# Performance work log

Hardware: AMD Instinct MI355X
Metric: run time of the kernel (lower is better)

## Reference

```python
import math
import jax, jax.numpy as jnp
import numpy as np

B, T, D, K, R, KC = 4, 2048, 1024, 8, 16, 4
H = 4 * D  # mlp hidden


def setup_inputs() -> dict:
    key = jax.random.key(0)
    ks = jax.random.split(key, 12)
    s = lambda i, shape: jax.random.normal(ks[i], shape, jnp.float32) * 0.02
    # state_decay_logit init: geometric decays in [dmin, dmax], logit = log(p) - log1p(-p)
    dmin, dmax = 0.9, 0.999
    dec = np.exp(np.linspace(math.log(dmin), math.log(dmax), K))
    decay_logit = jnp.asarray(np.log(dec) - np.log1p(-dec), jnp.float32)
    return dict(
        x=jax.random.normal(ks[0], (B, T, D), jnp.float32),
        conv_w=s(1, (D, 1, KC)),            # depthwise conv kernel (torch Conv1d weight)
        gp_w=s(2, (D, D)), gp_b=jnp.zeros((D,), jnp.float32),
        up_w=s(3, (D, H)), up_b=jnp.zeros((H,), jnp.float32),
        dn_w=s(4, (H, D)), dn_b=jnp.zeros((D,), jnp.float32),
        si_w=s(5, (D, K * D)),              # state_in (no bias)
        so_w=s(6, (K * D, D)),              # state_out (no bias)
        decay_logit=decay_logit,
        rs_w=s(7, (D, R)), rs_b=jnp.zeros((R,), jnp.float32),
        rwg_w=s(8, (D, 1)), rwg_b=jnp.zeros((1,), jnp.float32),
        rv_w=s(9, (D, D)), rv_b=jnp.zeros((D,), jnp.float32),
        gr_w=s(10, (D, 1)), gr_b=jnp.zeros((1,), jnp.float32),
        gl_w=s(11, (D, 1)), gl_b=jnp.zeros((1,), jnp.float32),
    )


def _rms_norm(x, eps=1e-6):
    return x * jax.lax.rsqrt(jnp.mean(x * x, axis=-1, keepdims=True) + eps)


def _forward(x, conv_w, gp_w, gp_b, up_w, up_b, dn_w, dn_b, si_w, so_w,
             decay_logit, rs_w, rs_b, rwg_w, rwg_b, rv_w, rv_b, gr_w, gr_b, gl_w, gl_b):
    Bx, Tx, Dx = x.shape
    u = _rms_norm(x)
    # --- local mixer: causal depthwise conv + sigmoid gate + SiLU MLP ---
    xc = jax.lax.conv_general_dilated(
        jnp.swapaxes(u, 1, 2), conv_w, window_strides=(1,),
        padding=[(KC - 1, 0)], feature_group_count=Dx,
        dimension_numbers=('NCH', 'OIH', 'NCH'))
    xc = jnp.swapaxes(xc, 1, 2)                       # (B,T,D) causal conv output
    xg = xc * jax.nn.sigmoid(xc @ gp_w + gp_b)
    local = jax.nn.silu(xg @ up_w + up_b) @ dn_w + dn_b
    # --- per-channel exponential-decay state + register read/write scan ---
    dec = jax.nn.sigmoid(decay_logit)                 # (K,)
    z = (u @ si_w).reshape(Bx, Tx, K, Dx)             # state_in, (B,T,K,D)
    sel = jax.nn.softmax(u @ rs_w + rs_b, axis=-1)    # soft register address (B,T,R)
    wg = jax.nn.sigmoid(u @ rwg_w + rwg_b)            # write gate (B,T,1)
    v = u @ rv_w + rv_b                                # register value (B,T,D)

    def step(carry, inp):
        s, regs = carry
        z_t, sel_t, w_t, v_t = inp
        read = jnp.einsum('br,brd->bd', sel_t, regs)  # soft read before write
        ws = (w_t * sel_t)[:, :, None]                # (B,R,1)
        regs = regs * (1.0 - ws) + ws * v_t[:, None, :]
        s = dec[None, :, None] * s + z_t
        return (s, regs), (s, read)

    init = (jnp.zeros((Bx, K, Dx), x.dtype), jnp.zeros((Bx, R, Dx), x.dtype))
    tm = lambda a: jnp.swapaxes(a, 0, 1)              # time-major for scan
    _, (s_all, reads) = jax.lax.scan(step, init, (tm(z), tm(sel), tm(wg), tm(v)))
    s_all = tm(s_all)                                 # (B,T,K,D)
    reads = tm(reads)                                 # (B,T,D)
    long_out = jnp.einsum('btkd,kde->bte', s_all, so_w.reshape(K, Dx, Dx))
    g_long = jax.nn.sigmoid(u @ gl_w + gl_b)
    g_reg = jax.nn.sigmoid(u @ gr_w + gr_b)
    return x + local + g_long * long_out + g_reg * reads


def reference(x, conv_w, gp_w, gp_b, up_w, up_b, dn_w, dn_b, si_w, so_w,
              decay_logit, rs_w, rs_b, rwg_w, rwg_b, rv_w, rv_b, gr_w, gr_b, gl_w, gl_b):
    return _forward(x, conv_w, gp_w, gp_b, up_w, up_b, dn_w, dn_b, si_w, so_w,
                    decay_logit, rs_w, rs_b, rwg_w, rwg_b, rv_w, rv_b, gr_w, gr_b, gl_w, gl_b)
```

## Files before the change

### kernel.cpp

```cpp
#include <hip/hip_runtime.h>

typedef unsigned short u16;
typedef __bf16 bf16x8 __attribute__((ext_vector_type(8)));
typedef float f32x4 __attribute__((ext_vector_type(4)));

#define D_ 1024
#define T_ 2048
#define B_ 4
#define K_ 8
#define R_ 16
#define H_ 4096
#define NROW (B_*T_)
#define CH 32
#define CL (T_/CH)

__device__ __forceinline__ u16 f2bf(float f){
  union{float f;unsigned u;} v; v.f=f;
  unsigned r = v.u + 0x7FFFu + ((v.u>>16)&1u);
  return (u16)(r>>16);
}
__device__ __forceinline__ float bf2f(u16 b){
  union{unsigned u;float f;} v; v.u = ((unsigned)b)<<16; return v.f;
}
__device__ __forceinline__ float sigm(float x){ return 1.f/(1.f+__expf(-x)); }

__device__ __forceinline__ void gload_lds16(const void* g, void* l){
  __builtin_amdgcn_global_load_lds((const __attribute__((address_space(1))) void*)g,
                                   (__attribute__((address_space(3))) void*)l, 16, 0, 0);
}

__global__ __launch_bounds__(256) void fill_k(float* __restrict__ out, long n, float v){
  long i = (long)blockIdx.x*256 + threadIdx.x;
  if (i < n) out[i] = v;
}

__global__ __launch_bounds__(256) void transpose_cast(const float* __restrict__ in, u16* __restrict__ out,
                                                      int R, int C){
  __shared__ float tile[32][33];
  int bx = blockIdx.x*32;
  int by = blockIdx.y*32;
  int tx = threadIdx.x & 31, ty = threadIdx.x >> 5;
  #pragma unroll
  for (int i=0;i<32;i+=8) tile[ty+i][tx] = in[(size_t)(by+ty+i)*C + bx+tx];
  __syncthreads();
  #pragma unroll
  for (int i=0;i<32;i+=8) out[(size_t)(bx+ty+i)*R + by+tx] = f2bf(tile[tx][ty+i]);
}

__global__ __launch_bounds__(256) void castbf(const float* __restrict__ in, u16* __restrict__ out, long n){
  long i = (long)blockIdx.x*256 + threadIdx.x;
  if (i < n) out[i] = f2bf(in[i]);
}

__global__ __launch_bounds__(256) void rmsnorm_k(const float* __restrict__ x, u16* __restrict__ u){
  int row = blockIdx.x;
  const float* xr = x + (size_t)row*D_;
  float xv[4]; float ss = 0.f;
  #pragma unroll
  for (int i=0;i<4;i++){ xv[i] = xr[threadIdx.x + 256*i]; ss += xv[i]*xv[i]; }
  #pragma unroll
  for (int o=32;o>0;o>>=1) ss += __shfl_down(ss, o);
  __shared__ float red[4];
  if ((threadIdx.x&63)==0) red[threadIdx.x>>6] = ss;
  __syncthreads();
  float tot = red[0]+red[1]+red[2]+red[3];
  float r = rsqrtf(tot*(1.f/D_) + 1e-6f);
  #pragma unroll
  for (int i=0;i<4;i++) u[(size_t)row*D_ + threadIdx.x + 256*i] = f2bf(xv[i]*r);
}

__global__ __launch_bounds__(256) void conv_k(const u16* __restrict__ u, const float* __restrict__ w,
                                              u16* __restrict__ xc){
  size_t i = (size_t)blockIdx.x*256 + threadIdx.x;
  int d = (int)(i & (D_-1));
  int t = (int)((i >> 10) & (T_-1));
  float acc = 0.f;
  #pragma unroll
  for (int j=0;j<4;j++){
    int tt = t-3+j;
    if (tt >= 0) acc += bf2f(u[i + (size_t)(long)(j-3)*D_]) * w[d*4+j];
  }
  xc[i] = f2bf(acc);
}

__global__ __launch_bounds__(256) void smalln_k(const u16* __restrict__ u,
    const float* __restrict__ rs_w, const float* __restrict__ rs_b,
    const float* __restrict__ rwg_w, const float* __restrict__ rwg_b,
    const float* __restrict__ gl_w, const float* __restrict__ gl_b,
    const float* __restrict__ gr_w, const float* __restrict__ gr_b,
    float* __restrict__ sel, float* __restrict__ wg, float* __restrict__ gl, float* __restrict__ gr){
  int row = blockIdx.x, tid = threadIdx.x;
  float p[19];
  #pragma unroll
  for (int c=0;c<19;c++) p[c] = 0.f;
  for (int i=0;i<4;i++){
    int e = tid + i*256;
    float ue = bf2f(u[(size_t)row*D_ + e]);
    const float* rw = rs_w + (size_t)e*16;
    #pragma unroll
    for (int r=0;r<16;r++) p[r] += ue*rw[r];
    p[16] += ue*rwg_w[e];
    p[17] += ue*gl_w[e];
    p[18] += ue*gr_w[e];
  }
  __shared__ float red[19*4];
  #pragma unroll
  for (int c=0;c<19;c++){
    float v = p[c];
    #pragma unroll
    for (int o=32;o>0;o>>=1) v += __shfl_down(v, o);
    if ((tid&63)==0) red[c*4 + (tid>>6)] = v;
  }
  __syncthreads();
  if (tid==0){
    float s[19];
    #pragma unroll
    for (int c=0;c<19;c++) s[c] = red[c*4]+red[c*4+1]+red[c*4+2]+red[c*4+3];
    float mx = -1e30f;
    #pragma unroll
    for (int r=0;r<16;r++){ s[r] += rs_b[r]; mx = fmaxf(mx, s[r]); }
    float ssum = 0.f;
    #pragma unroll
    for (int r=0;r<16;r++){ s[r] = __expf(s[r]-mx); ssum += s[r]; }
    float inv = 1.f/ssum;
    #pragma unroll
    for (int r=0;r<16;r++) sel[(size_t)row*16+r] = s[r]*inv;
    wg[row] = sigm(s[16] + rwg_b[0]);
    gl[row] = sigm(s[17] + gl_b[0]);
    gr[row] = sigm(s[18] + gr_b[0]);
  }
}

#define BM 128
#define BN 128
#define BK 32

template<int EPI>
__global__ __launch_bounds__(256)
void gemm_bt(const u16* __restrict__ A, const u16* __restrict__ BT,
             void* __restrict__ outp, const float* __restrict__ bias,
             const void* __restrict__ aux,
             int K, int lda, int ldb, int ldc,
             long zA, long zB, long zC)
{
  __shared__ __attribute__((aligned(16))) u16 As[BM*BK];
  __shared__ __attribute__((aligned(16))) u16 Bs[BN*BK];
  int nwg = gridDim.x*gridDim.y;
  int bx = blockIdx.x, by = blockIdx.y;
  if ((nwg & 7) == 0){
    int bid = blockIdx.y*gridDim.x + blockIdx.x;
    int cpx = nwg >> 3;
    int s = (bid & 7)*cpx + (bid >> 3);
    bx = s % gridDim.x; by = s / gridDim.x;
  }
  const u16* Ab = A + (size_t)blockIdx.z*zA + (size_t)bx*BM*lda;
  const u16* Bb = BT + (size_t)blockIdx.z*zB + (size_t)by*BN*ldb;
  int tid = threadIdx.x, lane = tid&63, wid = tid>>6;
  int wr = wid>>1, wc = wid&1;
  f32x4 acc[4][4];
  #pragma unroll
  for (int m=0;m<4;m++)
    #pragma unroll
    for (int n=0;n<4;n++) acc[m][n] = (f32x4){0.f,0.f,0.f,0.f};

  int srow = lane>>2;
  int scol = (lane&3)*8;
  int klo  = (lane>>4)*8;
  for (int k0=0; k0<K; k0+=BK){
    #pragma unroll
    for (int i=0;i<2;i++){
      int r0 = wid*32 + i*16;
      gload_lds16(Ab + (size_t)(r0+srow)*lda + k0 + scol, &As[r0*BK]);
      gload_lds16(Bb + (size_t)(r0+srow)*ldb + k0 + scol, &Bs[r0*BK]);
    }
    __syncthreads();
    bf16x8 af[4], bfr[4];
    #pragma unroll
    for (int m=0;m<4;m++) af[m] = *(const bf16x8*)&As[(wr*64+m*16+(lane&15))*BK + klo];
    #pragma unroll
    for (int n=0;n<4;n++) bfr[n] = *(const bf16x8*)&Bs[(wc*64+n*16+(lane&15))*BK + klo];
    #pragma unroll
    for (int m=0;m<4;m++)
      #pragma unroll
      for (int n=0;n<4;n++)
        acc[m][n] = __builtin_amdgcn_mfma_f32_16x16x32_bf16(af[m], bfr[n], acc[m][n], 0, 0, 0);
    __syncthreads();
  }

  size_t obase = (size_t)blockIdx.z*zC;
  int row0 = bx*BM + wr*64;
  int col0 = by*BN + wc*64;
  #pragma unroll
  for (int m=0;m<4;m++){
    #pragma unroll
    for (int n=0;n<4;n++){
      int col = col0 + n*16 + (lane&15);
      #pragma unroll
      for (int r=0;r<4;r++){
        int row = row0 + m*16 + (lane>>4)*4 + r;
        float c = acc[m][n][r];
        size_t idx = obase + (size_t)row*ldc + col;
        if (EPI==0){ ((u16*)outp)[idx] = f2bf(c); }
        else if (EPI==1){ ((u16*)outp)[idx] = f2bf(c + bias[col]); }
        else if (EPI==2){ float t=c+bias[col]; ((u16*)outp)[idx] = f2bf(bf2f(((const u16*)aux)[idx]) * sigm(t)); }
        else if (EPI==3){ float t=c+bias[col]; ((u16*)outp)[idx] = f2bf(t*sigm(t)); }
        else if (EPI==4){ ((float*)outp)[idx] = ((const float*)aux)[idx] + c + bias[col]; }
        else            { ((float*)outp)[idx] += c; }
      }
    }
  }
}

#define NT8 16

template<int EPI>
__global__ __launch_bounds__(512, 2)
void gemm8p(const u16* __restrict__ A, const u16* __restrict__ BT,
            void* __restrict__ outp, const float* __restrict__ bias,
            int lda, int ldb, int ldc)
{
  __shared__ __attribute__((aligned(16))) u16 lds8[65536];
  int nwg = gridDim.x*gridDim.y;
  int bid = blockIdx.y*gridDim.x + blockIdx.x;
  int cpx = nwg >> 3;
  int swz = (bid & 7)*cpx + (bid >> 3);
  int bx = swz % gridDim.x, by = swz / gridDim.x;

  const u16* Ab = A + (size_t)bx*256*lda;
  const u16* Bb = BT + (size_t)by*256*ldb;

  int tid = threadIdx.x, l = tid&63, w = tid>>6;
  int wr = w>>2, wc = w&3;
  int rS0 = (w*2+0)*8 + (l>>3);
  int rS1 = (w*2+1)*8 + (l>>3);
  int cg  = (((l&7) ^ (l>>3)) << 3);
  int seg0 = (w*2+0)*512;
  int seg1 = (w*2+1)*512;

  auto STAGE = [&](int h){
    int kt = h>>2, idx = h&3, par = kt&1;
    int koff = kt*64;
    if (idx < 2){
      const u16* s0 = Bb + (size_t)(idx*128 + rS0)*ldb + koff + cg;
      const u16* s1 = Bb + (size_t)(idx*128 + rS1)*ldb + koff + cg;
      u16* d = &lds8[par*32768 + 16384 + idx*8192];
      gload_lds16(s0, d + seg0);
      gload_lds16(s1, d + seg1);
    } else {
      int a = idx-2;
      const u16* s0 = Ab + (size_t)(a*128 + rS0)*lda + koff + cg;
      const u16* s1 = Ab + (size_t)(a*128 + rS1)*lda + koff + cg;
      u16* d = &lds8[par*32768 + a*8192];
      gload_lds16(s0, d + seg0);
      gload_lds16(s1, d + seg1);
    }
  };

  f32x4 acc[8][4];
  #pragma unroll
  for (int m=0;m<8;m++)
    #pragma unroll
    for (int n=0;n<4;n++) acc[m][n] = (f32x4){0.f,0.f,0.f,0.f};

  for (int h=0; h<7; ++h) STAGE(h);
  asm volatile("s_waitcnt vmcnt(6)" ::: "memory");
  __builtin_amdgcn_s_barrier();

  for (int it=0; it<NT8/2; ++it){
    #pragma unroll
    for (int sub=0; sub<2; ++sub){
      int kt = it*2+sub;
      const int par = sub;
      u16* Abase = &lds8[par*32768 + wr*8192];
      u16* Bbase = &lds8[par*32768 + 16384 + (wc>>1)*8192];
      bf16x8 bf[4][2];
      #pragma unroll
      for (int q=0; q<4; ++q){
        bf16x8 af[2][2];
        if (q==0){
          #pragma unroll
          for (int n=0;n<4;n++)
            #pragma unroll
            for (int s=0;s<2;s++){
              int rr = (wc&1)*64 + n*16 + (l&15);
              int c16 = (l>>4) + s*4;
              bf[n][s] = *(const bf16x8*)&Bbase[rr*64 + ((c16 ^ (rr&7))<<3)];
            }
        }
        #pragma unroll
        for (int i=0;i<2;i++)
          #pragma unroll
          for (int s=0;s<2;s++){
            int rr = q*32 + i*16 + (l&15);
            int c16 = (l>>4) + s*4;
            af[i][s] = *(const bf16x8*)&Abase[rr*64 + ((c16 ^ (rr&7))<<3)];
          }
        __builtin_amdgcn_sched_barrier(0);
        int h = kt*4 + q + 7;
        if (h < 4*NT8) STAGE(h);
        __builtin_amdgcn_s_barrier();
        asm volatile("s_waitcnt lgkmcnt(0)" ::: "memory");
        __builtin_amdgcn_sched_barrier(0);
        __builtin_amdgcn_s_setprio(1);
        #pragma unroll
        for (int i=0;i<2;i++)
          #pragma unroll
          for (int n=0;n<4;n++)
            #pragma unroll
            for (int s=0;s<2;s++)
              acc[q*2+i][n] = __builtin_amdgcn_mfma_f32_16x16x32_bf16(af[i][s], bf[n][s], acc[q*2+i][n], 0, 0, 0);
        __builtin_amdgcn_s_setprio(0);
        if (q==3){
          if (kt == NT8-2)      asm volatile("s_waitcnt vmcnt(0)" ::: "memory");
          else if (kt < NT8-2)  asm volatile("s_waitcnt vmcnt(6)" ::: "memory");
        }
        __builtin_amdgcn_s_barrier();
      }
    }
  }

  int row0 = bx*256 + wr*128;
  int col0 = by*256 + wc*64;
  #pragma unroll
  for (int m=0;m<8;m++){
    #pragma unroll
    for (int n=0;n<4;n++){
      int col = col0 + n*16 + (l&15);
      #pragma unroll
      for (int r=0;r<4;r++){
        int row = row0 + m*16 + (l>>4)*4 + r;
        float c = acc[m][n][r];
        size_t idx = (size_t)row*ldc + col;
        if (EPI==0){ ((u16*)outp)[idx] = f2bf(c); }
        else if (EPI==3){ float t=c+bias[col]; ((u16*)outp)[idx] = f2bf(t*sigm(t)); }
      }
    }
  }
}

template<int KH>
__global__ __launch_bounds__(256) void scan_s1t(const u16* __restrict__ y, const float* __restrict__ logit,
                                                int p, float* __restrict__ Hend){
  int e = blockIdx.x*256 + threadIdx.x;
  int c = blockIdx.y, b = blockIdx.z;
  float dec[KH], h[KH];
  #pragma unroll
  for (int k=0;k<KH;k++){ dec[k] = sigm(logit[KH*p+k]); h[k] = 0.f; }
  size_t row0 = (size_t)b*T_ + (size_t)c*CL;
  for (int t=0;t<CL;t++){
    const u16* yp = y + (row0+t)*(size_t)(KH*D_) + e;
    #pragma unroll
    for (int k=0;k<KH;k++) h[k] = dec[k]*h[k] + bf2f(yp[(size_t)k*D_]);
  }
  #pragma unroll
  for (int k=0;k<KH;k++) Hend[(((size_t)b*CH+c)*KH+k)*D_ + e] = h[k];
}

template<int KH>
__global__ __launch_bounds__(256) void scan_s2t(const float* __restrict__ Hend, const float* __restrict__ logit,
                                                int p, float* __restrict__ Sinit){
  int idx = blockIdx.x*256 + threadIdx.x;
  if (idx >= B_*KH*D_) return;
  int e = idx % D_; int kh = (idx/D_) % KH; int b = idx/(D_*KH);
  float dec = sigm(logit[KH*p+kh]);
  float dL = powf(dec, (float)CL);
  float carry = 0.f;
  for (int c=0;c<CH;c++){
    size_t i3 = (((size_t)b*CH+c)*KH+kh)*D_ + e;
    Sinit[i3] = carry;
    carry = dL*carry + Hend[i3];
  }
}

template<int KH>
__global__ __launch_bounds__(256) void scan_s3t(const u16* __restrict__ y, const float* __restrict__ logit,
                                                int p, const float* __restrict__ Sinit,
                                                const float* __restrict__ glb, float* __restrict__ out){
  int e = blockIdx.x*256 + threadIdx.x;
  int c = blockIdx.y, b = blockIdx.z;
  float dec[KH], h[KH];
  #pragma unroll
  for (int k=0;k<KH;k++){
    dec[k] = sigm(logit[KH*p+k]);
    h[k] = Sinit[(((size_t)b*CH+c)*KH+k)*D_ + e];
  }
  size_t row0 = (size_t)b*T_ + (size_t)c*CL;
  for (int t=0;t<CL;t++){
    const u16* yp = y + (row0+t)*(size_t)(KH*D_) + e;
    float sum = 0.f;
    #pragma unroll
    for (int k=0;k<KH;k++){ h[k] = dec[k]*h[k] + bf2f(yp[(size_t)k*D_]); sum += h[k]; }
    out[(row0+t)*D_ + e] += glb[row0+t] * sum;
  }
}

__global__ __launch_bounds__(256) void scan_r1(const u16* __restrict__ v, const float* __restrict__ sel,
                                               const float* __restrict__ wg,
                                               float* __restrict__ Rend, float* __restrict__ Pout){
  int d = blockIdx.x*256 + threadIdx.x;
  int c = blockIdx.y, b = blockIdx.z;
  __shared__ float sel_s[CL*R_];
  __shared__ float wg_s[CL];
  size_t row0 = (size_t)b*T_ + (size_t)c*CL;
  for (int i=threadIdx.x; i<CL*R_; i+=256) sel_s[i] = sel[row0*R_ + i];
  for (int i=threadIdx.x; i<CL;    i+=256) wg_s[i]  = wg[row0 + i];
  __syncthreads();
  float regs[R_], P[R_];
  #pragma unroll
  for (int r=0;r<R_;r++){ regs[r]=0.f; P[r]=1.f; }
  for (int t=0;t<CL;t++){
    float vv = bf2f(v[(row0+t)*D_ + d]);
    float w = wg_s[t];
    #pragma unroll
    for (int r=0;r<R_;r++){
      float ws = w*sel_s[t*R_+r];
      regs[r] += ws*(vv - regs[r]);
      P[r] *= (1.f - ws);
    }
  }
  #pragma unroll
  for (int r=0;r<R_;r++) Rend[(((size_t)b*CH+c)*R_+r)*D_ + d] = regs[r];
  if (blockIdx.x==0 && threadIdx.x==0){
    #pragma unroll
    for (int r=0;r<R_;r++) Pout[((size_t)b*CH+c)*R_ + r] = P[r];
  }
}

__global__ __launch_bounds__(256) void scan_r2(const float* __restrict__ Rend, const float* __restrict__ Pbuf,
                                               float* __restrict__ Rinit){
  int idx = blockIdx.x*256 + threadIdx.x;
  if (idx >= B_*D_) return;
  int d = idx % D_; int b = idx / D_;
  float regs[R_];
  #pragma unroll
  for (int r=0;r<R_;r++) regs[r] = 0.f;
  for (int c=0;c<CH;c++){
    #pragma unroll
    for (int r=0;r<R_;r++){
      size_t i3 = (((size_t)b*CH+c)*R_+r)*D_ + d;
      Rinit[i3] = regs[r];
      regs[r] = Pbuf[((size_t)b*CH+c)*R_+r]*regs[r] + Rend[i3];
    }
  }
}

__global__ __launch_bounds__(256) void scan_r3(const u16* __restrict__ v, const float* __restrict__ sel,
                                               const float* __restrict__ wg, const float* __restrict__ Rinit,
                                               const float* __restrict__ grb, float* __restrict__ out){
  int d = blockIdx.x*256 + threadIdx.x;
  int c = blockIdx.y, b = blockIdx.z;
  __shared__ float sel_s[CL*R_];
  __shared__ float wg_s[CL];
  size_t row0 = (size_t)b*T_ + (size_t)c*CL;
  for (int i=threadIdx.x; i<CL*R_; i+=256) sel_s[i] = sel[row0*R_ + i];
  for (int i=threadIdx.x; i<CL;    i+=256) wg_s[i]  = wg[row0 + i];
  __syncthreads();
  float regs[R_];
  #pragma unroll
  for (int r=0;r<R_;r++) regs[r] = Rinit[(((size_t)b*CH+c)*R_+r)*D_ + d];
  for (int t=0;t<CL;t++){
    float vv = bf2f(v[(row0+t)*D_ + d]);
    float w = wg_s[t];
    float read = 0.f;
    #pragma unroll
    for (int r=0;r<R_;r++){
      float sr = sel_s[t*R_+r];
      read += sr*regs[r];
      float ws = w*sr;
      regs[r] += ws*(vv - regs[r]);
    }
    out[(row0+t)*D_ + d] += grb[row0+t]*read;
  }
}

static void launch_gemm(int epi, dim3 g, const u16* A, const u16* BT, void* out,
                        const float* bias, const void* aux, int K, int lda, int ldb, int ldc,
                        long zA, long zB, long zC, hipStream_t s){
  switch(epi){
    case 0: gemm_bt<0><<<g,256,0,s>>>(A,BT,out,bias,aux,K,lda,ldb,ldc,zA,zB,zC); break;
    case 1: gemm_bt<1><<<g,256,0,s>>>(A,BT,out,bias,aux,K,lda,ldb,ldc,zA,zB,zC); break;
    case 2: gemm_bt<2><<<g,256,0,s>>>(A,BT,out,bias,aux,K,lda,ldb,ldc,zA,zB,zC); break;
    case 3: gemm_bt<3><<<g,256,0,s>>>(A,BT,out,bias,aux,K,lda,ldb,ldc,zA,zB,zC); break;
    case 4: gemm_bt<4><<<g,256,0,s>>>(A,BT,out,bias,aux,K,lda,ldb,ldc,zA,zB,zC); break;
    default: gemm_bt<5><<<g,256,0,s>>>(A,BT,out,bias,aux,K,lda,ldb,ldc,zA,zB,zC); break;
  }
}

extern "C" void kernel_launch(void* const* d_in, const int* in_sizes, int n_in,
                              void* d_out, int out_size, void* d_ws, size_t ws_size,
                              hipStream_t stream){
  const float* x      = (const float*)d_in[0];
  const float* conv_w = (const float*)d_in[1];
  const float* gp_w   = (const float*)d_in[2];
  const float* gp_b   = (const float*)d_in[3];
  const float* up_w   = (const float*)d_in[4];
  const float* up_b   = (const float*)d_in[5];
  const float* dn_w   = (const float*)d_in[6];
  const float* dn_b   = (const float*)d_in[7];
  const float* si_w   = (const float*)d_in[8];
  const float* so_w   = (const float*)d_in[9];
  const float* logit  = (const float*)d_in[10];
  const float* rs_w   = (const float*)d_in[11];
  const float* rs_b   = (const float*)d_in[12];
  const float* rwg_w  = (const float*)d_in[13];
  const float* rwg_b  = (const float*)d_in[14];
  const float* rv_w   = (const float*)d_in[15];
  const float* rv_b   = (const float*)d_in[16];
  const float* gr_w   = (const float*)d_in[17];
  const float* gr_b   = (const float*)d_in[18];
  const float* gl_w   = (const float*)d_in[19];
  const float* gl_b   = (const float*)d_in[20];
  float* out = (float*)d_out;
  char* base = (char*)d_ws;

  {
    size_t off = 0;
    auto al = [&](size_t b)->char*{ char* r = base+off; off += (b+255)&~(size_t)255; return r; };
    char* u_r    = al((size_t)NROW*D_*2);
    char* v_r    = al((size_t)NROW*D_*2);
    char* big    = al((size_t)121634816);
    float* sel   = (float*)al((size_t)NROW*R_*4);
    float* wgb   = (float*)al((size_t)NROW*4);
    float* glb   = (float*)al((size_t)NROW*4);
    float* grb   = (float*)al((size_t)NROW*4);
    float* Pbuf  = (float*)al((size_t)B_*CH*R_*4);
    float* Hend  = (float*)al((size_t)B_*CH*4*D_*4);
    float* Sinit = (float*)al((size_t)B_*CH*4*D_*4);
    float* Rend  = (float*)al((size_t)B_*CH*R_*D_*4);
    float* Rinit = (float*)al((size_t)B_*CH*R_*D_*4);
    if (off <= ws_size){
      u16* u_bf  = (u16*)u_r;
      u16* v_bf  = (u16*)v_r;
      u16* hid   = (u16*)big;
      u16* xc_bf = (u16*)(big + (size_t)67108864);
      u16* xg_bf = (u16*)(big + (size_t)83886080);
      u16* gpT   = (u16*)(big + (size_t)100663296);
      u16* upT   = (u16*)(big + (size_t)102760448);
      u16* dnT   = (u16*)(big + (size_t)111149056);
      u16* rvT   = (u16*)(big + (size_t)119537664);
      u16* WT    = (u16*)big;
      u16* si_bf = (u16*)(big + (size_t)16777216);
      u16* soT   = (u16*)(big + (size_t)33554432);
      u16* y_bf  = (u16*)(big + (size_t)16777216);

      transpose_cast<<<dim3(D_/32, D_/32),256,0,stream>>>(gp_w, gpT, D_, D_);
      transpose_cast<<<dim3(H_/32, D_/32),256,0,stream>>>(up_w, upT, D_, H_);
      transpose_cast<<<dim3(D_/32, H_/32),256,0,stream>>>(dn_w, dnT, H_, D_);
      transpose_cast<<<dim3(D_/32, D_/32),256,0,stream>>>(rv_w, rvT, D_, D_);

      rmsnorm_k<<<NROW,256,0,stream>>>(x, u_bf);
      conv_k<<<(NROW*D_)/256,256,0,stream>>>(u_bf, conv_w, xc_bf);
      smalln_k<<<NROW,256,0,stream>>>(u_bf, rs_w, rs_b, rwg_w, rwg_b, gl_w, gl_b, gr_w, gr_b,
                                      sel, wgb, glb, grb);

      launch_gemm(2, dim3(NROW/BM, D_/BN, 1), xc_bf, gpT, xg_bf, gp_b, xc_bf,
                  D_, D_, D_, D_, 0, 0, 0, stream);
      gemm8p<3><<<dim3(NROW/256, H_/256), 512, 0, stream>>>(xg_bf, upT, hid, up_b, D_, D_, H_);
      launch_gemm(4, dim3(NROW/BM, D_/BN, 1), hid, dnT, out, dn_b, x,
                  H_, H_, H_, D_, 0, 0, 0, stream);
      launch_gemm(1, dim3(NROW/BM, D_/BN, 1), u_bf, rvT, v_bf, rv_b, nullptr,
                  D_, D_, D_, D_, 0, 0, 0, stream);

      transpose_cast<<<dim3(D_/32, (K_*D_)/32),256,0,stream>>>(so_w, soT, K_*D_, D_);
      castbf<<<((long)D_*K_*D_+255)/256,256,0,stream>>>(si_w, si_bf, (long)D_*K_*D_);
      launch_gemm(0, dim3(D_/BM, D_/BN, K_), soT, si_bf, WT, nullptr, nullptr,
                  D_, K_*D_, K_*D_, D_, (long)D_, (long)D_, (long)D_*D_, stream);

      for (int h=0; h<2; h++){
        gemm8p<0><<<dim3(NROW/256, (4*D_)/256), 512, 0, stream>>>(
            u_bf, WT + (size_t)h*4*D_*D_, y_bf, nullptr, D_, D_, 4*D_);
        scan_s1t<4><<<dim3(D_/256, CH, B_),256,0,stream>>>(y_bf, logit, h, Hend);
        scan_s2t<4><<<(B_*4*D_+255)/256,256,0,stream>>>(Hend, logit, h, Sinit);
        scan_s3t<4><<<dim3(D_/256, CH, B_),256,0,stream>>>(y_bf, logit, h, Sinit, glb, out);
      }

      scan_r1<<<dim3(D_/256, CH, B_),256,0,stream>>>(v_bf, sel, wgb, Rend, Pbuf);
      scan_r2<<<(B_*D_+255)/256,256,0,stream>>>(Rend, Pbuf, Rinit);
      scan_r3<<<dim3(D_/256, CH, B_),256,0,stream>>>(v_bf, sel, wgb, Rinit, grb, out);
      return;
    }
  }

  const size_t MB16_8 = (size_t)NROW*D_*2;
  size_t off = 0;
  auto alloc = [&](size_t bytes)->char*{
    char* r = base + off; off += (bytes + 255) & ~(size_t)255; return r;
  };
  char* R0 = alloc(MB16_8);
  char* R1 = alloc(MB16_8);
  char* R2 = alloc(2*MB16_8);
  char* R3 = alloc((size_t)21*1024*1024);
  float* sel  = (float*)alloc((size_t)NROW*R_*4);
  float* wgb  = (float*)alloc((size_t)NROW*4);
  float* glb  = (float*)alloc((size_t)NROW*4);
  float* grb  = (float*)alloc((size_t)NROW*4);
  float* Pbuf = (float*)alloc((size_t)B_*CH*R_*4);
  float* Hend = (float*)alloc((size_t)B_*CH*2*D_*4);
  float* Sinit= (float*)alloc((size_t)B_*CH*2*D_*4);
  if (off > ws_size){
    fill_k<<<((long)out_size+255)/256,256,0,stream>>>(out, out_size, 12345.0f);
    return;
  }

  u16* u_bf  = (u16*)R0;
  u16* v_bf  = (u16*)R1;
  u16* xc_bf = (u16*)R2;
  u16* xg_bf = (u16*)(R2 + MB16_8);
  u16* hid_bf= (u16*)R2;
  u16* soT   = (u16*)R2;
  u16* si_bf = (u16*)(R2 + MB16_8);
  u16* y_bf  = (u16*)R2;
  u16* gpT   = (u16*)R3;
  u16* upT   = (u16*)(R3 + (size_t)2*1024*1024 + 131072);
  u16* dnT   = (u16*)(R3 + (size_t)10*1024*1024 + 655360);
  u16* rvT   = (u16*)(R3 + (size_t)19*1024*1024);
  u16* WT    = (u16*)R3;
  float* Rend = (float*)R3;
  float* Rinit= (float*)(R3 + (size_t)NROW*D_);

  transpose_cast<<<dim3(D_/32, D_/32),256,0,stream>>>(gp_w, gpT, D_, D_);
  transpose_cast<<<dim3(H_/32, D_/32),256,0,stream>>>(up_w, upT, D_, H_);
  transpose_cast<<<dim3(D_/32, H_/32),256,0,stream>>>(dn_w, dnT, H_, D_);
  transpose_cast<<<dim3(D_/32, D_/32),256,0,stream>>>(rv_w, rvT, D_, D_);

  rmsnorm_k<<<NROW,256,0,stream>>>(x, u_bf);
  conv_k<<<(NROW*D_)/256,256,0,stream>>>(u_bf, conv_w, xc_bf);
  smalln_k<<<NROW,256,0,stream>>>(u_bf, rs_w, rs_b, rwg_w, rwg_b, gl_w, gl_b, gr_w, gr_b,
                                  sel, wgb, glb, grb);

  launch_gemm(2, dim3(NROW/BM, D_/BN, 1), xc_bf, gpT, xg_bf, gp_b, xc_bf,
              D_, D_, D_, D_, 0, 0, 0, stream);
  launch_gemm(1, dim3(NROW/BM, D_/BN, 1), u_bf, rvT, v_bf, rv_b, nullptr,
              D_, D_, D_, D_, 0, 0, 0, stream);
  for (int q=0; q<4; q++){
    launch_gemm(3, dim3(NROW/BM, 1024/BN, 1), xg_bf, upT + (size_t)q*1024*D_, hid_bf,
                up_b + q*1024, nullptr, D_, D_, D_, 1024, 0, 0, 0, stream);
    launch_gemm(q==0?4:5, dim3(NROW/BM, D_/BN, 1), hid_bf, dnT + (size_t)q*1024, out,
                dn_b, x, 1024, 1024, H_, D_, 0, 0, 0, stream);
  }

  transpose_cast<<<dim3(D_/32, (K_*D_)/32),256,0,stream>>>(so_w, soT, K_*D_, D_);
  castbf<<<((long)D_*K_*D_+255)/256,256,0,stream>>>(si_w, si_bf, (long)D_*K_*D_);
  launch_gemm(0, dim3(D_/BM, D_/BN, K_), soT, si_bf, WT, nullptr, nullptr,
              D_, K_*D_, K_*D_, D_, (long)D_, (long)D_, (long)D_*D_, stream);

  for (int p=0; p<4; p++){
    launch_gemm(0, dim3(NROW/BM, (2*D_)/BN, 1), u_bf, WT + (size_t)(2*p)*D_*D_, y_bf,
                nullptr, nullptr, D_, D_, D_, 2*D_, 0, 0, 0, stream);
    scan_s1t<2><<<dim3(D_/256, CH, B_),256,0,stream>>>(y_bf, logit, p, Hend);
    scan_s2t<2><<<(B_*2*D_+255)/256,256,0,stream>>>(Hend, logit, p, Sinit);
    scan_s3t<2><<<dim3(D_/256, CH, B_),256,0,stream>>>(y_bf, logit, p, Sinit, glb, out);
  }

  scan_r1<<<dim3(D_/256, CH, B_),256,0,stream>>>(v_bf, sel, wgb, Rend, Pbuf);
  scan_r2<<<(B_*D_+255)/256,256,0,stream>>>(Rend, Pbuf, Rinit);
  scan_r3<<<dim3(D_/256, CH, B_),256,0,stream>>>(v_bf, sel, wgb, Rinit, grb, out);
}
```

Before: 770.8 us.

## Route all GEMMs through 256x256 kernel, split-K down-proj with atomics, vectorize scans

```diff
diff --git a/kernel.cpp b/kernel.cpp
--- a/kernel.cpp
+++ b/kernel.cpp
@@ -3,6 +3,7 @@
 typedef unsigned short u16;
 typedef __bf16 bf16x8 __attribute__((ext_vector_type(8)));
 typedef float f32x4 __attribute__((ext_vector_type(4)));
+typedef u16 u16x4 __attribute__((ext_vector_type(4)));
 
 #define D_ 1024
 #define T_ 2048
@@ -13,6 +14,8 @@
 #define NROW (B_*T_)
 #define CH 32
 #define CL (T_/CH)
+#define CHS 64
+#define CLS (T_/CHS)
 
 __device__ __forceinline__ u16 f2bf(float f){
   union{float f;unsigned u;} v; v.f=f;
@@ -52,6 +55,15 @@
   if (i < n) out[i] = f2bf(in[i]);
 }
 
+__global__ __launch_bounds__(256) void initout_k(const float* __restrict__ x, const float* __restrict__ b,
+                                                 float* __restrict__ out){
+  size_t i = ((size_t)blockIdx.x*256 + threadIdx.x)*4;
+  f32x4 xv = *(const f32x4*)(x + i);
+  f32x4 bv = *(const f32x4*)(b + (i & (D_-1)));
+  xv += bv;
+  *(f32x4*)(out + i) = xv;
+}
+
 __global__ __launch_bounds__(256) void rmsnorm_k(const float* __restrict__ x, u16* __restrict__ u){
   int row = blockIdx.x;
   const float* xr = x + (size_t)row*D_;
@@ -71,16 +83,25 @@
 
 __global__ __launch_bounds__(256) void conv_k(const u16* __restrict__ u, const float* __restrict__ w,
                                               u16* __restrict__ xc){
-  size_t i = (size_t)blockIdx.x*256 + threadIdx.x;
-  int d = (int)(i & (D_-1));
-  int t = (int)((i >> 10) & (T_-1));
-  float acc = 0.f;
+  size_t base = ((size_t)blockIdx.x*256 + threadIdx.x)*4;
+  int t  = (int)((base >> 10) & (T_-1));
+  int d0 = (int)(base & (D_-1));
+  f32x4 wv[4];
+  #pragma unroll
+  for (int jj=0;jj<4;jj++) wv[jj] = *(const f32x4*)&w[(d0+jj)*4];
+  float acc[4] = {0.f,0.f,0.f,0.f};
   #pragma unroll
   for (int j=0;j<4;j++){
-    int tt = t-3+j;
-    if (tt >= 0) acc += bf2f(u[i + (size_t)(long)(j-3)*D_]) * w[d*4+j];
-  }
-  xc[i] = f2bf(acc);
+    if (t-3+j >= 0){
+      u16x4 uv = *(const u16x4*)(u + base + (long)(j-3)*D_);
+      #pragma unroll
+      for (int jj=0;jj<4;jj++) acc[jj] += bf2f(uv[jj]) * wv[jj][j];
+    }
+  }
+  u16x4 o;
+  #pragma unroll
+  for (int jj=0;jj<4;jj++) o[jj] = f2bf(acc[jj]);
+  *(u16x4*)(xc + base) = o;
 }
 
 __global__ __launch_bounds__(256) void smalln_k(const u16* __restrict__ u,
@@ -211,13 +232,12 @@
   }
 }
 
-#define NT8 16
-
-template<int EPI>
+template<int NT, int EPI>
 __global__ __launch_bounds__(512, 2)
 void gemm8p(const u16* __restrict__ A, const u16* __restrict__ BT,
             void* __restrict__ outp, const float* __restrict__ bias,
-            int lda, int ldb, int ldc)
+            const void* __restrict__ aux,
+            int lda, int ldb, int ldc, long zA, long zB, long zC)
 {
   __shared__ __attribute__((aligned(16))) u16 lds8[65536];
   int nwg = gridDim.x*gridDim.y;
@@ -226,8 +246,8 @@
   int swz = (bid & 7)*cpx + (bid >> 3);
   int bx = swz % gridDim.x, by = swz / gridDim.x;
 
-  const u16* Ab = A + (size_t)bx*256*lda;
-  const u16* Bb = BT + (size_t)by*256*ldb;
+  const u16* Ab = A + (size_t)blockIdx.z*zA + (size_t)bx*256*lda;
+  const u16* Bb = BT + (size_t)blockIdx.z*zB + (size_t)by*256*ldb;
 
   int tid = threadIdx.x, l = tid&63, w = tid>>6;
   int wr = w>>2, wc = w&3;
@@ -266,7 +286,7 @@
   asm volatile("s_waitcnt vmcnt(6)" ::: "memory");
   __builtin_amdgcn_s_barrier();
 
-  for (int it=0; it<NT8/2; ++it){
+  for (int it=0; it<NT/2; ++it){
     #pragma unroll
     for (int sub=0; sub<2; ++sub){
       int kt = it*2+sub;
@@ -297,7 +317,7 @@
           }
         __builtin_amdgcn_sched_barrier(0);
         int h = kt*4 + q + 7;
-        if (h < 4*NT8) STAGE(h);
+        if (h < 4*NT) STAGE(h);
         __builtin_amdgcn_s_barrier();
         asm volatile("s_waitcnt lgkmcnt(0)" ::: "memory");
         __builtin_amdgcn_sched_barrier(0);
@@ -311,14 +331,15 @@
               acc[q*2+i][n] = __builtin_amdgcn_mfma_f32_16x16x32_bf16(af[i][s], bf[n][s], acc[q*2+i][n], 0, 0, 0);
         __builtin_amdgcn_s_setprio(0);
         if (q==3){
-          if (kt == NT8-2)      asm volatile("s_waitcnt vmcnt(0)" ::: "memory");
-          else if (kt < NT8-2)  asm volatile("s_waitcnt vmcnt(6)" ::: "memory");
+          if (kt == NT-2)      asm volatile("s_waitcnt vmcnt(0)" ::: "memory");
+          else if (kt < NT-2)  asm volatile("s_waitcnt vmcnt(6)" ::: "memory");
         }
         __builtin_amdgcn_s_barrier();
       }
     }
   }
 
+  size_t obase = (size_t)blockIdx.z*zC;
   int row0 = bx*256 + wr*128;
   int col0 = by*256 + wc*64;
   #pragma unroll
@@ -330,67 +351,84 @@
       for (int r=0;r<4;r++){
         int row = row0 + m*16 + (l>>4)*4 + r;
         float c = acc[m][n][r];
-        size_t idx = (size_t)row*ldc + col;
+        size_t idx = obase + (size_t)row*ldc + col;
         if (EPI==0){ ((u16*)outp)[idx] = f2bf(c); }
+        else if (EPI==1){ ((u16*)outp)[idx] = f2bf(c + bias[col]); }
+        else if (EPI==2){ float t=c+bias[col]; ((u16*)outp)[idx] = f2bf(bf2f(((const u16*)aux)[idx]) * sigm(t)); }
         else if (EPI==3){ float t=c+bias[col]; ((u16*)outp)[idx] = f2bf(t*sigm(t)); }
+        else            { unsafeAtomicAdd(&((float*)outp)[idx], c); }
       }
     }
   }
 }
 
 template<int KH>
-__global__ __launch_bounds__(256) void scan_s1t(const u16* __restrict__ y, const float* __restrict__ logit,
+__global__ __launch_bounds__(256) void scan_s1v(const u16* __restrict__ y, const float* __restrict__ logit,
                                                 int p, float* __restrict__ Hend){
-  int e = blockIdx.x*256 + threadIdx.x;
+  int e0 = threadIdx.x*4;
   int c = blockIdx.y, b = blockIdx.z;
-  float dec[KH], h[KH];
-  #pragma unroll
-  for (int k=0;k<KH;k++){ dec[k] = sigm(logit[KH*p+k]); h[k] = 0.f; }
-  size_t row0 = (size_t)b*T_ + (size_t)c*CL;
-  for (int t=0;t<CL;t++){
-    const u16* yp = y + (row0+t)*(size_t)(KH*D_) + e;
-    #pragma unroll
-    for (int k=0;k<KH;k++) h[k] = dec[k]*h[k] + bf2f(yp[(size_t)k*D_]);
-  }
-  #pragma unroll
-  for (int k=0;k<KH;k++) Hend[(((size_t)b*CH+c)*KH+k)*D_ + e] = h[k];
+  float dec[KH]; f32x4 h[KH];
+  #pragma unroll
+  for (int k=0;k<KH;k++){ dec[k] = sigm(logit[KH*p+k]); h[k] = (f32x4){0.f,0.f,0.f,0.f}; }
+  size_t row0 = (size_t)b*T_ + (size_t)c*CLS;
+  for (int t=0;t<CLS;t++){
+    const u16* yp = y + (row0+t)*(size_t)(KH*D_) + e0;
+    #pragma unroll
+    for (int k=0;k<KH;k++){
+      u16x4 w = *(const u16x4*)(yp + (size_t)k*D_);
+      #pragma unroll
+      for (int j=0;j<4;j++) h[k][j] = dec[k]*h[k][j] + bf2f(w[j]);
+    }
+  }
+  #pragma unroll
+  for (int k=0;k<KH;k++)
+    *(f32x4*)&Hend[(((size_t)b*CHS+c)*KH+k)*D_ + e0] = h[k];
 }
 
 template<int KH>
-__global__ __launch_bounds__(256) void scan_s2t(const float* __restrict__ Hend, const float* __restrict__ logit,
+__global__ __launch_bounds__(256) void scan_s2v(const float* __restrict__ Hend, const float* __restrict__ logit,
                                                 int p, float* __restrict__ Sinit){
   int idx = blockIdx.x*256 + threadIdx.x;
   if (idx >= B_*KH*D_) return;
   int e = idx % D_; int kh = (idx/D_) % KH; int b = idx/(D_*KH);
   float dec = sigm(logit[KH*p+kh]);
-  float dL = powf(dec, (float)CL);
+  float dL = powf(dec, (float)CLS);
   float carry = 0.f;
-  for (int c=0;c<CH;c++){
-    size_t i3 = (((size_t)b*CH+c)*KH+kh)*D_ + e;
+  for (int c=0;c<CHS;c++){
+    size_t i3 = (((size_t)b*CHS+c)*KH+kh)*D_ + e;
     Sinit[i3] = carry;
     carry = dL*carry + Hend[i3];
   }
 }
 
 template<int KH>
-__global__ __launch_bounds__(256) void scan_s3t(const u16* __restrict__ y, const float* __restrict__ logit,
+__global__ __launch_bounds__(256) void scan_s3v(const u16* __restrict__ y, const float* __restrict__ logit,
                                                 int p, const float* __restrict__ Sinit,
                                                 const float* __restrict__ glb, float* __restrict__ out){
-  int e = blockIdx.x*256 + threadIdx.x;
+  int e0 = threadIdx.x*4;
   int c = blockIdx.y, b = blockIdx.z;
-  float dec[KH], h[KH];
+  float dec[KH]; f32x4 h[KH];
   #pragma unroll
   for (int k=0;k<KH;k++){
     dec[k] = sigm(logit[KH*p+k]);
-    h[k] = Sinit[(((size_t)b*CH+c)*KH+k)*D_ + e];
-  }
-  size_t row0 = (size_t)b*T_ + (size_t)c*CL;
-  for (int t=0;t<CL;t++){
-    const u16* yp = y + (row0+t)*(size_t)(KH*D_) + e;
-    float sum = 0.f;
-    #pragma unroll
-    for (int k=0;k<KH;k++){ h[k] = dec[k]*h[k] + bf2f(yp[(size_t)k*D_]); sum += h[k]; }
-    out[(row0+t)*D_ + e] += glb[row0+t] * sum;
+    h[k] = *(const f32x4*)&Sinit[(((size_t)b*CHS+c)*KH+k)*D_ + e0];
+  }
+  size_t row0 = (size_t)b*T_ + (size_t)c*CLS;
+  for (int t=0;t<CLS;t++){
+    const u16* yp = y + (row0+t)*(size_t)(KH*D_) + e0;
+    f32x4 sum = (f32x4){0.f,0.f,0.f,0.f};
+    #pragma unroll
+    for (int k=0;k<KH;k++){
+      u16x4 w = *(const u16x4*)(yp + (size_t)k*D_);
+      #pragma unroll
+      for (int j=0;j<4;j++){ h[k][j] = dec[k]*h[k][j] + bf2f(w[j]); sum[j] += h[k][j]; }
+    }
+    float g = glb[row0+t];
+    f32x4* op = (f32x4*)&out[(row0+t)*D_ + e0];
+    f32x4 ov = *op;
+    #pragma unroll
+    for (int j=0;j<4;j++) ov[j] += g*sum[j];
+    *op = ov;
   }
 }
 
@@ -524,8 +562,6 @@
     float* glb   = (float*)al((size_t)NROW*4);
     float* grb   = (float*)al((size_t)NROW*4);
     float* Pbuf  = (float*)al((size_t)B_*CH*R_*4);
-    float* Hend  = (float*)al((size_t)B_*CH*4*D_*4);
-    float* Sinit = (float*)al((size_t)B_*CH*4*D_*4);
     float* Rend  = (float*)al((size_t)B_*CH*R_*D_*4);
     float* Rinit = (float*)al((size_t)B_*CH*R_*D_*4);
     if (off <= ws_size){
@@ -542,6 +578,8 @@
       u16* si_bf = (u16*)(big + (size_t)16777216);
       u16* soT   = (u16*)(big + (size_t)33554432);
       u16* y_bf  = (u16*)(big + (size_t)16777216);
+      float* Hend  = (float*)(big + (size_t)83886080);
+      float* Sinit = (float*)(big + (size_t)88080384);
 
       transpose_cast<<<dim3(D_/32, D_/32),256,0,stream>>>(gp_w, gpT, D_, D_);
       transpose_cast<<<dim3(H_/32, D_/32),256,0,stream>>>(up_w, upT, D_, H_);
@@ -549,29 +587,31 @@
       transpose_cast<<<dim3(D_/32, D_/32),256,0,stream>>>(rv_w, rvT, D_, D_);
 
       rmsnorm_k<<<NROW,256,0,stream>>>(x, u_bf);
-      conv_k<<<(NROW*D_)/256,256,0,stream>>>(u_bf, conv_w, xc_bf);
+      conv_k<<<(NROW*D_)/1024,256,0,stream>>>(u_bf, conv_w, xc_bf);
       smalln_k<<<NROW,256,0,stream>>>(u_bf, rs_w, rs_b, rwg_w, rwg_b, gl_w, gl_b, gr_w, gr_b,
                                       sel, wgb, glb, grb);
 
-      launch_gemm(2, dim3(NROW/BM, D_/BN, 1), xc_bf, gpT, xg_bf, gp_b, xc_bf,
-                  D_, D_, D_, D_, 0, 0, 0, stream);
-      gemm8p<3><<<dim3(NROW/256, H_/256), 512, 0, stream>>>(xg_bf, upT, hid, up_b, D_, D_, H_);
-      launch_gemm(4, dim3(NROW/BM, D_/BN, 1), hid, dnT, out, dn_b, x,
-                  H_, H_, H_, D_, 0, 0, 0, stream);
-      launch_gemm(1, dim3(NROW/BM, D_/BN, 1), u_bf, rvT, v_bf, rv_b, nullptr,
-                  D_, D_, D_, D_, 0, 0, 0, stream);
+      gemm8p<16,2><<<dim3(NROW/256, D_/256), 512, 0, stream>>>(
+          xc_bf, gpT, xg_bf, gp_b, xc_bf, D_, D_, D_, 0, 0, 0);
+      gemm8p<16,3><<<dim3(NROW/256, H_/256), 512, 0, stream>>>(
+          xg_bf, upT, hid, up_b, nullptr, D_, D_, H_, 0, 0, 0);
+      initout_k<<<(NROW*D_)/1024,256,0,stream>>>(x, dn_b, out);
+      gemm8p<32,5><<<dim3(NROW/256, D_/256, 2), 512, 0, stream>>>(
+          hid, dnT, out, nullptr, nullptr, H_, H_, D_, 2048, 2048, 0);
+      gemm8p<16,1><<<dim3(NROW/256, D_/256), 512, 0, stream>>>(
+          u_bf, rvT, v_bf, rv_b, nullptr, D_, D_, D_, 0, 0, 0);
 
       transpose_cast<<<dim3(D_/32, (K_*D_)/32),256,0,stream>>>(so_w, soT, K_*D_, D_);
       castbf<<<((long)D_*K_*D_+255)/256,256,0,stream>>>(si_w, si_bf, (long)D_*K_*D_);
-      launch_gemm(0, dim3(D_/BM, D_/BN, K_), soT, si_bf, WT, nullptr, nullptr,
-                  D_, K_*D_, K_*D_, D_, (long)D_, (long)D_, (long)D_*D_, stream);
+      gemm8p<16,0><<<dim3(D_/256, D_/256, K_), 512, 0, stream>>>(
+          soT, si_bf, WT, nullptr, nullptr, K_*D_, K_*D_, D_, (long)D_, (long)D_, (long)D_*D_);
 
       for (int h=0; h<2; h++){
-        gemm8p<0><<<dim3(NROW/256, (4*D_)/256), 512, 0, stream>>>(
-            u_bf, WT + (size_t)h*4*D_*D_, y_bf, nullptr, D_, D_, 4*D_);
-        scan_s1t<4><<<dim3(D_/256, CH, B_),256,0,stream>>>(y_bf, logit, h, Hend);
-        scan_s2t<4><<<(B_*4*D_+255)/256,256,0,stream>>>(Hend, logit, h, Sinit);
-        scan_s3t<4><<<dim3(D_/256, CH, B_),256,0,stream>>>(y_bf, logit, h, Sinit, glb, out);
+        gemm8p<16,0><<<dim3(NROW/256, (4*D_)/256), 512, 0, stream>>>(
+            u_bf, WT + (size_t)h*4*D_*D_, y_bf, nullptr, nullptr, D_, D_, 4*D_, 0, 0, 0);
+        scan_s1v<4><<<dim3(1, CHS, B_),256,0,stream>>>(y_bf, logit, h, Hend);
+        scan_s2v<4><<<(B_*4*D_+255)/256,256,0,stream>>>(Hend, logit, h, Sinit);
+        scan_s3v<4><<<dim3(1, CHS, B_),256,0,stream>>>(y_bf, logit, h, Sinit, glb, out);
       }
 
       scan_r1<<<dim3(D_/256, CH, B_),256,0,stream>>>(v_bf, sel, wgb, Rend, Pbuf);
@@ -595,8 +635,8 @@
   float* glb  = (float*)alloc((size_t)NROW*4);
   float* grb  = (float*)alloc((size_t)NROW*4);
   float* Pbuf = (float*)alloc((size_t)B_*CH*R_*4);
-  float* Hend = (float*)alloc((size_t)B_*CH*2*D_*4);
-  float* Sinit= (float*)alloc((size_t)B_*CH*2*D_*4);
+  float* Hend = (float*)alloc((size_t)B_*CHS*2*D_*4);
+  float* Sinit= (float*)alloc((size_t)B_*CHS*2*D_*4);
   if (off > ws_size){
     fill_k<<<((long)out_size+255)/256,256,0,stream>>>(out, out_size, 12345.0f);
     return;
@@ -624,7 +664,7 @@
   transpose_cast<<<dim3(D_/32, D_/32),256,0,stream>>>(rv_w, rvT, D_, D_);
 
   rmsnorm_k<<<NROW,256,0,stream>>>(x, u_bf);
-  conv_k<<<(NROW*D_)/256,256,0,stream>>>(u_bf, conv_w, xc_bf);
+  conv_k<<<(NROW*D_)/1024,256,0,stream>>>(u_bf, conv_w, xc_bf);
   smalln_k<<<NROW,256,0,stream>>>(u_bf, rs_w, rs_b, rwg_w, rwg_b, gl_w, gl_b, gr_w, gr_b,
                                   sel, wgb, glb, grb);
 
@@ -647,9 +687,9 @@
   for (int p=0; p<4; p++){
     launch_gemm(0, dim3(NROW/BM, (2*D_)/BN, 1), u_bf, WT + (size_t)(2*p)*D_*D_, y_bf,
                 nullptr, nullptr, D_, D_, D_, 2*D_, 0, 0, 0, stream);
-    scan_s1t<2><<<dim3(D_/256, CH, B_),256,0,stream>>>(y_bf, logit, p, Hend);
-    scan_s2t<2><<<(B_*2*D_+255)/256,256,0,stream>>>(Hend, logit, p, Sinit);
-    scan_s3t<2><<<dim3(D_/256, CH, B_),256,0,stream>>>(y_bf, logit, p, Sinit, glb, out);
+    scan_s1v<2><<<dim3(1, CHS, B_),256,0,stream>>>(y_bf, logit, p, Hend);
+    scan_s2v<2><<<(B_*2*D_+255)/256,256,0,stream>>>(Hend, logit, p, Sinit);
+    scan_s3v<2><<<dim3(1, CHS, B_),256,0,stream>>>(y_bf, logit, p, Sinit, glb, out);
   }
 
   scan_r1<<<dim3(D_/256, CH, B_),256,0,stream>>>(v_bf, sel, wgb, Rend, Pbuf);
```

Measured after the change: 726.0 us. 1.06x faster.
